# Kernel tuning notes

Measured on AMD Instinct MI355X. Metric: run time of the kernel, lower is better.

## Reference

```python
import jax, jax.numpy as jnp
import numpy as np

NUM_SEGMENTS = 16

def setup_inputs() -> dict:
    key = jax.random.key(0)
    k1, k2, k3, k4 = jax.random.split(key, 4)
    C, R = 256, 4
    x = jax.random.normal(k1, (1000000, C), dtype=jnp.float32)
    indices = jax.random.randint(k2, (1000000,), 0, NUM_SEGMENTS, dtype=jnp.int64)
    # Linear weights (torch Linear: y = x @ W.T); store as (in, out) for einsum
    w1 = jax.random.normal(k3, (C, C // R), dtype=jnp.float32) / np.sqrt(C)
    w2 = jax.random.normal(k4, (C // R, C), dtype=jnp.float32) / np.sqrt(C // R)
    return {"x": x, "indices": indices, "w1": w1, "w2": w2}

def reference(x, indices, w1, w2):
    idx = indices.astype(jnp.int32)
    # scatter-mean over segments: (S, C)
    seg_sum = jax.ops.segment_sum(x, idx, num_segments=NUM_SEGMENTS)
    counts = jax.ops.segment_sum(jnp.ones((x.shape[0],), x.dtype), idx, num_segments=NUM_SEGMENTS)
    seg_mean = seg_sum / jnp.maximum(counts, 1.0)[:, None]
    # tiny SE MLP: Linear -> ReLU -> Linear -> Sigmoid
    h = jax.nn.relu(seg_mean @ w1)
    gate = jax.nn.sigmoid(h @ w2)  # (S, C)
    # gather per-point gate and modulate
    return x * gate[idx]
```

## Files before the change

kernel.cpp:

```cpp
#include <hip/hip_runtime.h>
#include <math.h>

#define C 256
#define S 16
#define CR 64
#define NREP 8

__global__ __launch_bounds__(128) void k_segsum(
    const float* __restrict__ x, const int* __restrict__ idx,
    float* __restrict__ psum, int* __restrict__ pcnt, int nrows)
{
    __shared__ float ls[S][C];
    __shared__ int   lc[S];
    const int t = threadIdx.x;

    #pragma unroll
    for (int i = t; i < S * C; i += 128) (&ls[0][0])[i] = 0.0f;
    if (t < S) lc[t] = 0;
    __syncthreads();

    const float2* __restrict__ x2 = reinterpret_cast<const float2*>(x);
    for (int row = blockIdx.x; row < nrows; row += gridDim.x) {
        const int s = idx[row];
        float2 v = x2[row * (C / 2) + t];
        float2* p = reinterpret_cast<float2*>(&ls[s][2 * t]);
        float2 cur = *p;
        cur.x += v.x; cur.y += v.y;
        *p = cur;
        if (t == 0) lc[s]++;
    }
    __syncthreads();

    const int rep = blockIdx.x & (NREP - 1);
    float* gs = psum + rep * S * C;
    int*   gc = pcnt + rep * S;
    for (int i = t; i < S * C; i += 128) atomicAdd(&gs[i], (&ls[0][0])[i]);
    if (t < S) atomicAdd(&gc[t], lc[t]);
}

__global__ __launch_bounds__(256) void k_mlp(
    const float* __restrict__ psum, const int* __restrict__ pcnt,
    const float* __restrict__ w1, const float* __restrict__ w2,
    float* __restrict__ gate)
{
    __shared__ float sm[S][C];
    __shared__ float h[S][CR];
    __shared__ float cnt[S];
    const int t = threadIdx.x;

    if (t < S) {
        int c = 0;
        #pragma unroll
        for (int r = 0; r < NREP; r++) c += pcnt[r * S + t];
        cnt[t] = fmaxf((float)c, 1.0f);
    }
    __syncthreads();

    for (int i = t; i < S * C; i += 256) {
        float v = 0.0f;
        #pragma unroll
        for (int r = 0; r < NREP; r++) v += psum[r * S * C + i];
        sm[i / C][i % C] = v / cnt[i / C];
    }
    __syncthreads();

    for (int o = t; o < S * CR; o += 256) {
        const int s = o / CR, j = o % CR;
        float acc = 0.0f;
        #pragma unroll 4
        for (int k = 0; k < C; k++) acc += sm[s][k] * w1[k * CR + j];
        h[s][j] = fmaxf(acc, 0.0f);
    }
    __syncthreads();

    for (int o = t; o < S * C; o += 256) {
        const int s = o / C, j = o % C;
        float acc = 0.0f;
        #pragma unroll
        for (int k = 0; k < CR; k++) acc += h[s][k] * w2[k * C + j];
        gate[o] = 1.0f / (1.0f + expf(-acc));
    }
}

__global__ __launch_bounds__(256) void k_mod(
    const float* __restrict__ x, const int* __restrict__ idx,
    const float* __restrict__ gate, float* __restrict__ out, int nrows)
{
    const int l    = threadIdx.x & 63;
    const int wrow = threadIdx.x >> 6;
    const float4* __restrict__ x4 = reinterpret_cast<const float4*>(x);
    const float4* __restrict__ g4 = reinterpret_cast<const float4*>(gate);
    float4* __restrict__ o4 = reinterpret_cast<float4*>(out);

    for (int row = blockIdx.x * 4 + wrow; row < nrows; row += gridDim.x * 4) {
        const int s = idx[row];
        float4 v = x4[row * (C / 4) + l];
        const float4 g = g4[s * (C / 4) + l];
        v.x *= g.x; v.y *= g.y; v.z *= g.z; v.w *= g.w;
        o4[row * (C / 4) + l] = v;
    }
}

extern "C" void kernel_launch(void* const* d_in, const int* in_sizes, int n_in,
                              void* d_out, int out_size, void* d_ws, size_t ws_size,
                              hipStream_t stream)
{
    const float* x   = (const float*)d_in[0];
    const int*   idx = (const int*)  d_in[1];
    const float* w1  = (const float*)d_in[2];
    const float* w2  = (const float*)d_in[3];
    float* out = (float*)d_out;
    const int nrows = in_sizes[1];

    float* psum = (float*)d_ws;
    int*   pcnt = (int*)(psum + NREP * S * C);
    float* gate = (float*)(pcnt + NREP * S);

    const size_t zero_bytes = NREP * S * C * sizeof(float) + NREP * S * sizeof(int);
    hipMemsetAsync(d_ws, 0, zero_bytes, stream);

    k_segsum<<<2048, 128, 0, stream>>>(x, idx, psum, pcnt, nrows);
    k_mlp<<<1, 256, 0, stream>>>(psum, pcnt, w1, w2, gate);
    k_mod<<<2048, 256, 0, stream>>>(x, idx, gate, out, nrows);
}
```

Measured before the change: 768.5 us.

## Replace LDS segment histogram with per-wave register accumulation via ballots

The segment-sum kernel no longer keeps a shared-memory accumulator per block. Each wave owns four segments in registers, uses ballots to find rows in 64-row chunks that belong to those segments, and loads and accumulates only those rows with float4 loads, four at a time. Counts come from ballot popcounts and go to a single global counter array. The replica count for partial sums rises to spread atomics. This removes LDS read-modify-write traffic and per-row barrier-free serialization, at the cost of each wave reading the index array fully and doing masked FMAs for four segments.

```diff
diff --git a/kernel.cpp b/kernel.cpp
--- a/kernel.cpp
+++ b/kernel.cpp
@@ -4,38 +4,89 @@
 #define C 256
 #define S 16
 #define CR 64
-#define NREP 8
+#define NREP 16
 
-__global__ __launch_bounds__(128) void k_segsum(
+typedef float f4 __attribute__((ext_vector_type(4)));
+
+__global__ __launch_bounds__(256, 4) void k_segsum(
     const float* __restrict__ x, const int* __restrict__ idx,
     float* __restrict__ psum, int* __restrict__ pcnt, int nrows)
 {
-    __shared__ float ls[S][C];
-    __shared__ int   lc[S];
-    const int t = threadIdx.x;
+    const int lane = threadIdx.x & 63;
+    const int w    = threadIdx.x >> 6;
+    const int blk  = blockIdx.x;
+    const int nblk = gridDim.x;
 
-    #pragma unroll
-    for (int i = t; i < S * C; i += 128) (&ls[0][0])[i] = 0.0f;
-    if (t < S) lc[t] = 0;
-    __syncthreads();
+    f4 a0={0,0,0,0}, a1={0,0,0,0}, a2={0,0,0,0}, a3={0,0,0,0};
+    int c0=0, c1=0, c2=0, c3=0;
 
-    const float2* __restrict__ x2 = reinterpret_cast<const float2*>(x);
-    for (int row = blockIdx.x; row < nrows; row += gridDim.x) {
-        const int s = idx[row];
-        float2 v = x2[row * (C / 2) + t];
-        float2* p = reinterpret_cast<float2*>(&ls[s][2 * t]);
-        float2 cur = *p;
-        cur.x += v.x; cur.y += v.y;
-        *p = cur;
-        if (t == 0) lc[s]++;
+    const f4* __restrict__ x4 = reinterpret_cast<const f4*>(x);
+    const int nsb = (nrows + 63) >> 6;
+    const int base = w << 2;
+
+    #define ROW4(sv, hv, vv) { \
+        const float m0 = (sv == base + 0) ? hv : 0.0f; \
+        const float m1 = (sv == base + 1) ? hv : 0.0f; \
+        const float m2 = (sv == base + 2) ? hv : 0.0f; \
+        const float m3 = (sv == base + 3) ? hv : 0.0f; \
+        a0.x = fmaf(m0, vv.x, a0.x); a0.y = fmaf(m0, vv.y, a0.y); \
+        a0.z = fmaf(m0, vv.z, a0.z); a0.w = fmaf(m0, vv.w, a0.w); \
+        a1.x = fmaf(m1, vv.x, a1.x); a1.y = fmaf(m1, vv.y, a1.y); \
+        a1.z = fmaf(m1, vv.z, a1.z); a1.w = fmaf(m1, vv.w, a1.w); \
+        a2.x = fmaf(m2, vv.x, a2.x); a2.y = fmaf(m2, vv.y, a2.y); \
+        a2.z = fmaf(m2, vv.z, a2.z); a2.w = fmaf(m2, vv.w, a2.w); \
+        a3.x = fmaf(m3, vv.x, a3.x); a3.y = fmaf(m3, vv.y, a3.y); \
+        a3.z = fmaf(m3, vv.z, a3.z); a3.w = fmaf(m3, vv.w, a3.w); }
+
+    for (int sb = blk; sb < nsb; sb += nblk) {
+        const int row0 = sb << 6;
+        const bool valid = (row0 + lane) < nrows;
+        const int myseg = valid ? idx[row0 + lane] : -1;
+        unsigned long long m = __ballot((myseg >> 2) == w);
+
+        c0 += (int)__popcll(__ballot(myseg == base + 0));
+        c1 += (int)__popcll(__ballot(myseg == base + 1));
+        c2 += (int)__popcll(__ballot(myseg == base + 2));
+        c3 += (int)__popcll(__ballot(myseg == base + 3));
+
+        while (m) {
+            const int  b0 = (int)__ffsll((long long)m) - 1;  m &= m - 1;
+            const bool h1 = m != 0;
+            const int  b1 = h1 ? (int)__ffsll((long long)m) - 1 : b0;
+            if (h1) m &= m - 1;
+            const bool h2 = m != 0;
+            const int  b2 = h2 ? (int)__ffsll((long long)m) - 1 : b0;
+            if (h2) m &= m - 1;
+            const bool h3 = m != 0;
+            const int  b3 = h3 ? (int)__ffsll((long long)m) - 1 : b0;
+            if (h3) m &= m - 1;
+
+            const f4 v0 = x4[(size_t)(row0 + b0) * (C/4) + lane];
+            const f4 v1 = x4[(size_t)(row0 + b1) * (C/4) + lane];
+            const f4 v2 = x4[(size_t)(row0 + b2) * (C/4) + lane];
+            const f4 v3 = x4[(size_t)(row0 + b3) * (C/4) + lane];
+
+            const int s0 = __builtin_amdgcn_readlane(myseg, b0);
+            const int s1 = __builtin_amdgcn_readlane(myseg, b1);
+            const int s2 = __builtin_amdgcn_readlane(myseg, b2);
+            const int s3 = __builtin_amdgcn_readlane(myseg, b3);
+
+            ROW4(s0, 1.0f, v0)
+            ROW4(s1, h1 ? 1.0f : 0.0f, v1)
+            ROW4(s2, h2 ? 1.0f : 0.0f, v2)
+            ROW4(s3, h3 ? 1.0f : 0.0f, v3)
+        }
     }
-    __syncthreads();
+    #undef ROW4
 
-    const int rep = blockIdx.x & (NREP - 1);
-    float* gs = psum + rep * S * C;
-    int*   gc = pcnt + rep * S;
-    for (int i = t; i < S * C; i += 128) atomicAdd(&gs[i], (&ls[0][0])[i]);
-    if (t < S) atomicAdd(&gc[t], lc[t]);
+    const int rep = ((blk << 2) | w) & (NREP - 1);
+    float* gs = psum + (size_t)rep * S * C;
+    #define FLUSH(K) { float* fp = gs + (base + K) * C + 4 * lane; \
+        atomicAdd(fp + 0, a##K.x); atomicAdd(fp + 1, a##K.y); \
+        atomicAdd(fp + 2, a##K.z); atomicAdd(fp + 3, a##K.w); \
+        if (lane == 0 && c##K) atomicAdd(&pcnt[base + K], c##K); }
+    FLUSH(0) FLUSH(1) FLUSH(2) FLUSH(3)
+    #undef FLUSH
 }
 
 __global__ __launch_bounds__(256) void k_mlp(
@@ -48,12 +99,7 @@
     __shared__ float cnt[S];
     const int t = threadIdx.x;
 
-    if (t < S) {
-        int c = 0;
-        #pragma unroll
-        for (int r = 0; r < NREP; r++) c += pcnt[r * S + t];
-        cnt[t] = fmaxf((float)c, 1.0f);
-    }
+    if (t < S) cnt[t] = fmaxf((float)pcnt[t], 1.0f);
     __syncthreads();
 
     for (int i = t; i < S * C; i += 256) {
@@ -114,12 +160,12 @@
 
     float* psum = (float*)d_ws;
     int*   pcnt = (int*)(psum + NREP * S * C);
-    float* gate = (float*)(pcnt + NREP * S);
+    float* gate = (float*)(pcnt + S);
 
-    const size_t zero_bytes = NREP * S * C * sizeof(float) + NREP * S * sizeof(int);
-    hipMemsetAsync(d_ws, 0, zero_bytes, stream);
+    const size_t zero_bytes = NREP * S * C * sizeof(float) + S * sizeof(int);
+    (void)hipMemsetAsync(d_ws, 0, zero_bytes, stream);
 
-    k_segsum<<<2048, 128, 0, stream>>>(x, idx, psum, pcnt, nrows);
-    k_mlp<<<1, 256, 0, stream>>>(psum, pcnt, w1, w2, gate);
-    k_mod<<<2048, 256, 0, stream>>>(x, idx, gate, out, nrows);
+    k_segsum<<<1024, 256, 0, stream>>>(x, idx, psum, pcnt, nrows);
+    k_mlp   <<<   1, 256, 0, stream>>>(psum, pcnt, w1, w2, gate);
+    k_mod   <<<2048, 256, 0, stream>>>(x, idx, gate, out, nrows);
 }
```

Result: slower. 853.6 us (+11.1%).
